# Optimization experiments

Measured on AMD Instinct MI355X. Metric: run time of the kernel, lower is better.

The kernel has to match this reference:

```python
import jax, jax.numpy as jnp
import numpy as np

N, E, F, H, L, G, C, NC = 100000, 1200000, 32, 64, 3, 256, 200000, 10
D = L * H  # concat node embedding dim = 192


def setup_inputs() -> dict:
    key = jax.random.key(0)
    ks = jax.random.split(key, 20)

    def w(k, shape):
        fan_in = shape[-2] if len(shape) > 1 else shape[0]
        return jax.random.normal(k, shape, jnp.float32) * (1.0 / np.sqrt(fan_in))

    inp = dict(
        x=jax.random.normal(ks[0], (N, F), jnp.float32),
        edge_index=jax.random.randint(ks[1], (2, E), 0, N),
        batch=jnp.sort(jax.random.randint(ks[2], (N,), 0, G)),
        cand_node=jax.random.randint(ks[3], (C,), 0, N),
        c1_W1=w(ks[4], (F, H)), c1_b1=jnp.zeros((H,)),
        c1_W2=w(ks[5], (H, H)), c1_b2=jnp.zeros((H,)),
        c1_g=jnp.ones((H,)), c1_be=jnp.zeros((H,)), c1_m=jnp.zeros((H,)), c1_v=jnp.ones((H,)),
        c1_eps=jnp.zeros((1,)),
        cs_W1=w(ks[6], (L - 1, H, H)), cs_b1=jnp.zeros((L - 1, H)),
        cs_W2=w(ks[7], (L - 1, H, H)), cs_b2=jnp.zeros((L - 1, H)),
        cs_g=jnp.ones((L - 1, H)), cs_be=jnp.zeros((L - 1, H)),
        cs_m=jnp.zeros((L - 1, H)), cs_v=jnp.ones((L - 1, H)),
        cs_eps=jnp.zeros((L - 1,)),
        nc_W1=w(ks[8], (D, 2 * H)), nc_b1=jnp.zeros((2 * H,)),
        nc_W2=w(ks[9], (2 * H, H)), nc_b2=jnp.zeros((H,)),
        nc_W3=w(ks[10], (H, H)), nc_b3=jnp.zeros((H,)),
        nc_W4=w(ks[11], (H, NC)), nc_b4=jnp.zeros((NC,)),
        comp_emb=jax.random.normal(ks[12], (NC, D), jnp.float32),
        ep_W1=w(ks[13], (2 * D, 2 * H)), ep_b1=jnp.zeros((2 * H,)),
        ep_W2=w(ks[14], (2 * H, H)), ep_b2=jnp.zeros((H,)),
        ep_W3=w(ks[15], (H, 1)), ep_b3=jnp.zeros((1,)),
    )
    return inp


def _bn(h, g, b, m, v):
    # BatchNorm1d in eval mode with running stats
    return g * (h - m) * jax.lax.rsqrt(v + 1e-5) + b


def _gin_layer(h, src, dst, eps, W1, b1, W2, b2, g, be, m, v):
    agg = jax.ops.segment_sum(h[src], dst, num_segments=N)  # sum aggregation
    h = (1.0 + eps) * h + agg
    h = jax.nn.relu(h @ W1 + b1)
    h = jax.nn.relu(h @ W2 + b2)
    return _bn(h, g, be, m, v)


def reference(x, edge_index, batch, cand_node,
              c1_W1, c1_b1, c1_W2, c1_b2, c1_g, c1_be, c1_m, c1_v, c1_eps,
              cs_W1, cs_b1, cs_W2, cs_b2, cs_g, cs_be, cs_m, cs_v, cs_eps,
              nc_W1, nc_b1, nc_W2, nc_b2, nc_W3, nc_b3, nc_W4, nc_b4,
              comp_emb, ep_W1, ep_b1, ep_W2, ep_b2, ep_W3, ep_b3):
    src, dst = edge_index[0], edge_index[1]
    # shared GIN encoder: concat per-layer node embeddings -> [N, L*H]
    h = _gin_layer(x, src, dst, c1_eps, c1_W1, c1_b1, c1_W2, c1_b2, c1_g, c1_be, c1_m, c1_v)
    xs = [h]
    for i in range(cs_W1.shape[0]):
        h = _gin_layer(h, src, dst, cs_eps[i], cs_W1[i], cs_b1[i], cs_W2[i], cs_b2[i],
                       cs_g[i], cs_be[i], cs_m[i], cs_v[i])
        xs.append(h)
    node_emb = jnp.concatenate(xs, axis=-1)  # [N, D]

    # global mean pool per graph -> classification head (dropout=identity in eval)
    sums = jax.ops.segment_sum(node_emb, batch, num_segments=G)
    cnt = jax.ops.segment_sum(jnp.ones((node_emb.shape[0], 1), node_emb.dtype), batch, num_segments=G)
    graph_emb = sums / jnp.maximum(cnt, 1.0)  # [G, D]
    hc = jax.nn.relu(graph_emb @ nc_W1 + nc_b1)
    hc = jax.nn.relu(hc @ nc_W2 + nc_b2)
    hc = jax.nn.relu(hc @ nc_W3 + nc_b3)
    logits = hc @ nc_W4 + nc_b4
    class_output = jax.nn.log_softmax(logits, axis=-1)  # [G, NC]

    # link prediction: predicted comp type per graph, score all candidates in one batch
    comp_idx = jnp.argmax(class_output, axis=-1)          # [G]
    cand_graph = batch[cand_node]                          # [C]
    ce = comp_emb[comp_idx[cand_graph]]                    # [C, D]
    de = node_emb[cand_node]                               # [C, D]
    ef = jnp.concatenate([ce, de], axis=-1)                # [C, 2D]
    he = jax.nn.relu(ef @ ep_W1 + ep_b1)
    he = jax.nn.relu(he @ ep_W2 + ep_b2)
    edge_scores = jax.nn.sigmoid((he @ ep_W3 + ep_b3).squeeze(-1))  # [C]
    return class_output, edge_scores
```

## Files before the change

### kernel.cpp

```cpp
#include <hip/hip_runtime.h>
#include <hip/hip_bf16.h>


#define GG 256
#define NCC 10
#define DD 192
#define BSH 9

#define PE_BLK 133
#define EN_BLK 88
#define XB_BLK 512

typedef short bf16x8 __attribute__((ext_vector_type(8)));
typedef float f32x4  __attribute__((ext_vector_type(4)));

__device__ inline unsigned short f2bf_u(float x) {
    __hip_bfloat16 h = __float2bfloat16(x);
    return *reinterpret_cast<unsigned short*>(&h);
}
__device__ inline float bf2f(unsigned short u) {
    return __uint_as_float(((unsigned int)u) << 16);
}

__global__ void prep_all(
    const float* __restrict__ epW1, const float* __restrict__ epb1,
    const float* __restrict__ epW2, const float* __restrict__ comp_emb,
    unsigned short* __restrict__ W1b_p, unsigned short* __restrict__ W2_p,
    float* __restrict__ pc,
    const float* __restrict__ c1W1, const float* __restrict__ c1W2,
    const float* __restrict__ csW1, const float* __restrict__ csW2,
    unsigned short* __restrict__ enc,
    const float* __restrict__ x, unsigned short* __restrict__ xb, int nx4,
    int* __restrict__ bcnt, int* __restrict__ nbrpad) {
    const int b = blockIdx.x, t = threadIdx.x;
    if (b < PE_BLK) {
        int idx = b * 256 + t;
        const int S1 = 6 * 8 * 512;
        const int S2 = 4 * 4 * 512;
        if (idx < S1) {
            int frag = idx >> 9;
            int lane = (idx >> 3) & 63;
            int j = idx & 7;
            int kstep = frag >> 3, nt = frag & 7;
            int k = kstep * 32 + ((lane >> 4) << 3) + j;
            int n = nt * 16 + (lane & 15);
            W1b_p[idx] = f2bf_u(epW1[(192 + k) * 128 + n]);
        } else if (idx < S1 + S2) {
            int i2 = idx - S1;
            int frag = i2 >> 9;
            int lane = (i2 >> 3) & 63;
            int j = i2 & 7;
            int kstep = frag >> 2, nt = frag & 3;
            int k = kstep * 32 + ((lane >> 4) << 3) + j;
            int n = nt * 16 + (lane & 15);
            W2_p[i2] = f2bf_u(epW2[k * 64 + n]);
        } else if (idx < S1 + S2 + NCC * 128) {
            int i3 = idx - (S1 + S2);
            int ci = i3 >> 7, col = i3 & 127;
            float a = epb1[col];
            for (int k = 0; k < DD; ++k) a += comp_emb[ci * DD + k] * epW1[k * 128 + col];
            pc[i3] = a;
        }
    } else if (b < PE_BLK + EN_BLK) {
        int idx = (b - PE_BLK) * 256 + t;
        if (idx < 22528) {
            const float* W; int rel;
            if (idx < 2048)       { W = c1W1;        rel = idx; }
            else if (idx < 6144)  { W = c1W2;        rel = idx - 2048; }
            else if (idx < 10240) { W = csW1;        rel = idx - 6144; }
            else if (idx < 14336) { W = csW2;        rel = idx - 10240; }
            else if (idx < 18432) { W = csW1 + 4096; rel = idx - 14336; }
            else                  { W = csW2 + 4096; rel = idx - 18432; }
            int frag = rel >> 9;
            int lane = (rel >> 3) & 63;
            int j = rel & 7;
            int ks = frag >> 2, nt = frag & 3;
            int k = ks * 32 + ((lane >> 4) << 3) + j;
            int n = nt * 16 + (lane & 15);
            enc[idx] = f2bf_u(W[k * 64 + n]);
        }
    } else if (b < PE_BLK + EN_BLK + XB_BLK) {
        for (int i = (b - PE_BLK - EN_BLK) * 256 + t; i < nx4; i += XB_BLK * 256) {
            float4 v = *(const float4*)(x + i * 4);
            ushort4 u;
            u.x = f2bf_u(v.x); u.y = f2bf_u(v.y); u.z = f2bf_u(v.z); u.w = f2bf_u(v.w);
            *(ushort4*)(xb + i * 4) = u;
        }
    } else {
        bcnt[t] = 0; bcnt[t + 256] = 0;
        if (t < 128) nbrpad[t] = 0;
    }
}

__global__ void bin_hist(const int* __restrict__ dst, int* __restrict__ bcnt, int E_) {
    __shared__ int h[512];
    const int t = threadIdx.x;
    h[t] = 0; h[t + 256] = 0;
    __syncthreads();
    for (int e = blockIdx.x * 256 + t; e < E_; e += gridDim.x * 256)
        atomicAdd(&h[dst[e] >> BSH], 1);
    __syncthreads();
    if (h[t]) atomicAdd(&bcnt[t], h[t]);
    if (h[t + 256]) atomicAdd(&bcnt[t + 256], h[t + 256]);
}

__global__ void scan_misc(const int* __restrict__ bcnt, int* __restrict__ bbase,
                          int* __restrict__ bpos, int NB, int E_,
                          const int* __restrict__ batch, int* __restrict__ gcnt_i,
                          float* __restrict__ gsum, int N_) {
    const int b = blockIdx.x, t = threadIdx.x;
    if (b == 0) {
        __shared__ int ps[256];
        int v0 = (2 * t < NB) ? bcnt[2 * t] : 0;
        int v1 = (2 * t + 1 < NB) ? bcnt[2 * t + 1] : 0;
        int pv = v0 + v1;
        ps[t] = pv;
        __syncthreads();
        for (int off = 1; off < 256; off <<= 1) {
            int x = (t >= off) ? ps[t - off] : 0;
            __syncthreads();
            ps[t] += x;
            __syncthreads();
        }
        const int excl = ps[t] - pv;
        if (2 * t < NB)     { bbase[2 * t] = excl;          bpos[2 * t] = excl; }
        if (2 * t + 1 < NB) { bbase[2 * t + 1] = excl + v0; bpos[2 * t + 1] = excl + v0; }
        if (t == 0) bbase[NB] = E_;
    } else if (b == 1) {
        __shared__ int lbs[GG + 1];
        int lo = 0, hi = N_;
        while (lo < hi) {
            int mid = (lo + hi) >> 1;
            if (batch[mid] < t) lo = mid + 1; else hi = mid;
        }
        lbs[t] = lo;
        if (t == 0) lbs[GG] = N_;
        __syncthreads();
        gcnt_i[t] = lbs[t + 1] - lbs[t];
    } else {
        int i = (b - 2) * 256 + t;
        if (i < GG * DD) gsum[i] = 0.f;
    }
}

__global__ __launch_bounds__(256) void bin_scatter(
    const int* __restrict__ src, const int* __restrict__ dst,
    int* __restrict__ bpos, unsigned* __restrict__ ebuf, int E_) {
    __shared__ int h[512];
    __shared__ int base[512];
    const int t = threadIdx.x;
    const int e0 = blockIdx.x * 4096;
    h[t] = 0; h[t + 256] = 0;
    __syncthreads();
    int myb[16], myr[16];
    unsigned pk[16];
    #pragma unroll
    for (int u = 0; u < 16; ++u) {
        int e = e0 + t + u * 256;
        if (e < E_) {
            int d = dst[e];
            myb[u] = d >> BSH;
            pk[u] = ((unsigned)src[e] << BSH) | (unsigned)(d & ((1 << BSH) - 1));
            myr[u] = atomicAdd(&h[myb[u]], 1);
        } else myb[u] = -1;
    }
    __syncthreads();
    if (h[t]) base[t] = atomicAdd(&bpos[t], h[t]);
    if (h[t + 256]) base[t + 256] = atomicAdd(&bpos[t + 256], h[t + 256]);
    __syncthreads();
    #pragma unroll
    for (int u = 0; u < 16; ++u)
        if (myb[u] >= 0)
            ebuf[base[myb[u]] + myr[u]] = pk[u];
}

__global__ __launch_bounds__(256) void csr_bucket(
    const unsigned* __restrict__ ebuf, const int* __restrict__ bbase,
    int* __restrict__ rowptr, int* __restrict__ nbr, int N_, int NB) {
    __shared__ int lh[512];
    __shared__ int lx[512];
    __shared__ int ps[256];
    const int b = blockIdx.x;
    const int t = threadIdx.x;
    const int ebase = bbase[b], eend = bbase[b + 1];
    const int ecnt = eend - ebase;
    const int n0 = b << BSH;
    const unsigned M = (1 << BSH) - 1;

    for (int i = t; i < 512; i += 256) lh[i] = 0;
    __syncthreads();
    for (int i = t; i < ecnt; i += 256)
        atomicAdd(&lh[ebuf[ebase + i] & M], 1);
    __syncthreads();

    int pv = lh[2 * t] + lh[2 * t + 1];
    ps[t] = pv;
    __syncthreads();
    for (int off = 1; off < 256; off <<= 1) {
        int x = (t >= off) ? ps[t - off] : 0;
        __syncthreads();
        ps[t] += x;
        __syncthreads();
    }
    const int excl = ps[t] - pv;
    lx[2 * t] = excl;
    lx[2 * t + 1] = excl + lh[2 * t];
    __syncthreads();

    for (int i = t; i < 512; i += 256) {
        int n = n0 + i;
        if (n < N_) rowptr[n] = ebase + lx[i];
    }
    if (b == NB - 1 && t == 0) rowptr[N_] = eend;
    __syncthreads();
    for (int i = t; i < 512; i += 256) lh[i] = lx[i];
    __syncthreads();
    for (int i = t; i < ecnt; i += 256) {
        unsigned p = ebuf[ebase + i];
        int r = atomicAdd(&lh[p & M], 1);
        nbr[ebase + r] = (int)(p >> BSH);
    }
}

#define SWZ(row, byte) ((byte) ^ (((row) & 7) << 4))

#define GSTEP(VCUR, VNXT)                                                     \
    _Pragma("unroll")                                                         \
    for (int u = 0; u < 16; ++u)                                              \
        VNXT[u] = bf2f(*(const unsigned short*)(hbase + (unsigned)idx[u] * (unsigned)RSB + lane2)); \
    _Pragma("unroll")                                                         \
    for (int u = 0; u < 16; ++u) idx[u] = nbp[k + 32 + u];                    \
    {                                                                         \
        float runk = run;                                                     \
        _Pragma("unroll")                                                     \
        for (int u = 0; u < 16; ++u) run += VCUR[u];                          \
        if ((unsigned)(e1 - k) < 16u) { float tt = runk;                      \
            _Pragma("unroll")                                                 \
            for (int u = 0; u < 16; ++u) tt += (u < e1 - k) ? VCUR[u] : 0.f;  \
            s0 = tt; }                                                        \
        if ((unsigned)(e2 - k) < 16u) { float tt = runk;                      \
            _Pragma("unroll")                                                 \
            for (int u = 0; u < 16; ++u) tt += (u < e2 - k) ? VCUR[u] : 0.f;  \
            s1 = tt; }                                                        \
        if ((unsigned)(e3 - k) < 16u) { float tt = runk;                      \
            _Pragma("unroll")                                                 \
            for (int u = 0; u < 16; ++u) tt += (u < e3 - k) ? VCUR[u] : 0.f;  \
            s2 = tt; }                                                        \
        if ((unsigned)(cnt - k) < 16u) { float tt = runk;                     \
            _Pragma("unroll")                                                 \
            for (int u = 0; u < 16; ++u) tt += (u < cnt - k) ? VCUR[u] : 0.f; \
            s3 = tt; }                                                        \
    }                                                                         \
    k += 16;                                                                  \
    if (k > cnt) break;

template<int K>
__global__ __launch_bounds__(512) void gin_fused(
    const unsigned short* __restrict__ hin_b,
    const int* __restrict__ rowptr, const int* __restrict__ nbr,
    const unsigned short* __restrict__ W1p, const float* __restrict__ b1,
    const unsigned short* __restrict__ W2p, const float* __restrict__ b2,
    const float* __restrict__ gamma, const float* __restrict__ beta,
    const float* __restrict__ mean, const float* __restrict__ var,
    const float* __restrict__ eps_p,
    __hip_bfloat16* __restrict__ out_b,
    const int* __restrict__ batch, float* __restrict__ gsum, int soff,
    int N_) {
    __shared__ char s_agg[32 * 128];
    __shared__ char s_h1[32 * 128];
    __shared__ char s_out[32 * 128];
    __shared__ int sb[32];

    const int t = threadIdx.x;
    const int lane = t & 63;
    const int w = t >> 6;
    const int node0 = blockIdx.x * 32;
    const int nb = w * 4;

    if (t < 32) sb[t] = (node0 + t < N_) ? batch[node0 + t] : -1;

    const float eps1 = 1.0f + eps_p[0];

    const int n0w = node0 + nb;
    const int rp0 = __builtin_amdgcn_readfirstlane(rowptr[min(n0w + 0, N_)]);
    const int rp1 = __builtin_amdgcn_readfirstlane(rowptr[min(n0w + 1, N_)]);
    const int rp2 = __builtin_amdgcn_readfirstlane(rowptr[min(n0w + 2, N_)]);
    const int rp3 = __builtin_amdgcn_readfirstlane(rowptr[min(n0w + 3, N_)]);
    const int rp4 = __builtin_amdgcn_readfirstlane(rowptr[min(n0w + 4, N_)]);
    const int cnt = rp4 - rp0;
    const int e1 = rp1 - rp0, e2 = rp2 - rp0, e3 = rp3 - rp0;
    const int* nbp = nbr + rp0;

    const int RSB = (K == 64) ? DD * 2 : 64;
    const int OST = (K == 64) ? DD : 32;
    const char* hbase = (const char*)hin_b;
    const unsigned lane2 = (unsigned)(lane & (K - 1)) * 2u;

    int idx[16];
    float vA[16], vB[16];
    float run = 0.f, s0 = 0.f, s1 = 0.f, s2 = 0.f, s3 = 0.f;
    #pragma unroll
    for (int u = 0; u < 16; ++u) idx[u] = nbp[u];
    #pragma unroll
    for (int u = 0; u < 16; ++u)
        vA[u] = bf2f(*(const unsigned short*)(hbase + (unsigned)idx[u] * (unsigned)RSB + lane2));
    #pragma unroll
    for (int u = 0; u < 16; ++u) idx[u] = nbp[16 + u];
    for (int k = 0;;) {
        GSTEP(vA, vB)
        GSTEP(vB, vA)
    }
    float a0 = s0, a1 = s1 - s0, a2 = s2 - s1, a3 = s3 - s2;
    {
        const unsigned short* hbp = hin_b + (lane & (K - 1));
        if (n0w + 0 < N_) a0 += eps1 * bf2f(hbp[(size_t)(n0w + 0) * OST]);
        if (n0w + 1 < N_) a1 += eps1 * bf2f(hbp[(size_t)(n0w + 1) * OST]);
        if (n0w + 2 < N_) a2 += eps1 * bf2f(hbp[(size_t)(n0w + 2) * OST]);
        if (n0w + 3 < N_) a3 += eps1 * bf2f(hbp[(size_t)(n0w + 3) * OST]);
    }
    if (K == 64 || lane < 32) {
        const int kd = lane & (K - 1);
        *(unsigned short*)(s_agg + SWZ(nb + 0, (nb + 0) * 128 + kd * 2)) = f2bf_u(a0);
        *(unsigned short*)(s_agg + SWZ(nb + 1, (nb + 1) * 128 + kd * 2)) = f2bf_u(a1);
        *(unsigned short*)(s_agg + SWZ(nb + 2, (nb + 2) * 128 + kd * 2)) = f2bf_u(a2);
        *(unsigned short*)(s_agg + SWZ(nb + 3, (nb + 3) * 128 + kd * 2)) = f2bf_u(a3);
    }
    __syncthreads();

    const int mt = w >> 2, nt = w & 3;
    const int arow = mt * 16 + (lane & 15);
    const int col = nt * 16 + (lane & 15);
    f32x4 c1v = (f32x4){0.f, 0.f, 0.f, 0.f};
    #pragma unroll
    for (int ks = 0; ks < K / 32; ++ks) {
        bf16x8 a = *(const bf16x8*)(s_agg + SWZ(arow, arow * 128 + ks * 64 + ((lane >> 4) << 4)));
        bf16x8 b = *(const bf16x8*)(W1p + (((ks << 2) + nt) << 9) + (lane << 3));
        c1v = __builtin_amdgcn_mfma_f32_16x16x32_bf16(a, b, c1v, 0, 0, 0);
    }
    {
        const float bb1 = b1[col];
        #pragma unroll
        for (int reg = 0; reg < 4; ++reg) {
            int row = mt * 16 + ((lane >> 4) << 2) + reg;
            float v = fmaxf(c1v[reg] + bb1, 0.f);
            *(unsigned short*)(s_h1 + SWZ(row, row * 128 + col * 2)) = f2bf_u(v);
        }
    }
    __syncthreads();

    f32x4 c2v = (f32x4){0.f, 0.f, 0.f, 0.f};
    #pragma unroll
    for (int ks = 0; ks < 2; ++ks) {
        bf16x8 a = *(const bf16x8*)(s_h1 + SWZ(arow, arow * 128 + ks * 64 + ((lane >> 4) << 4)));
        bf16x8 b = *(const bf16x8*)(W2p + (((ks << 2) + nt) << 9) + (lane << 3));
        c2v = __builtin_amdgcn_mfma_f32_16x16x32_bf16(a, b, c2v, 0, 0, 0);
    }
    {
        const float bb2 = b2[col];
        const float ga = gamma[col], bet = beta[col], mu = mean[col];
        const float iv = rsqrtf(var[col] + 1e-5f);
        #pragma unroll
        for (int reg = 0; reg < 4; ++reg) {
            int row = mt * 16 + ((lane >> 4) << 2) + reg;
            float v = fmaxf(c2v[reg] + bb2, 0.f);
            v = ga * (v - mu) * iv + bet;
            *(unsigned short*)(s_out + SWZ(row, row * 128 + col * 2)) = f2bf_u(v);
        }
    }
    __syncthreads();

    {
        int r = t >> 4, c8 = t & 15;
        int node = node0 + r;
        if (node < N_) {
            ushort4 v = *(const ushort4*)(s_out + SWZ(r, r * 128 + c8 * 8));
            *(ushort4*)((unsigned short*)out_b + (size_t)node * DD + c8 * 4) = v;
        }
    }

    if (t < 256) {
        const int d = t & 63;
        const int rg = t >> 6;
        float acc = 0.f;
        int curg = sb[rg * 8];
        #pragma unroll
        for (int r = rg * 8; r < rg * 8 + 8; ++r) {
            int g = sb[r];
            if (g != curg) {
                if (curg >= 0) atomicAdd(&gsum[curg * DD + soff + d], acc);
                acc = 0.f; curg = g;
            }
            if (g >= 0)
                acc += bf2f(*(const unsigned short*)(s_out + SWZ(r, r * 128 + d * 2)));
        }
        if (curg >= 0) atomicAdd(&gsum[curg * DD + soff + d], acc);
    }
}

__global__ void head_kernel(const float* __restrict__ gsum, const int* __restrict__ gcnt_i,
                            const float* __restrict__ W1, const float* __restrict__ b1,
                            const float* __restrict__ W2, const float* __restrict__ b2,
                            const float* __restrict__ W3, const float* __restrict__ b3,
                            const float* __restrict__ W4, const float* __restrict__ b4,
                            float* __restrict__ class_out, int* __restrict__ comp_idx) {
    const int g = blockIdx.x;
    const int t = threadIdx.x;
    __shared__ float ge[DD], h1[128], h2[64], h3[64], logits[NCC];

    const float c = fmaxf((float)gcnt_i[g], 1.0f);
    if (t < DD) ge[t] = gsum[g * DD + t] / c;
    __syncthreads();

    if (t < 128) {
        float a = b1[t];
        #pragma unroll 4
        for (int k = 0; k < DD; ++k) a += ge[k] * W1[k * 128 + t];
        h1[t] = fmaxf(a, 0.0f);
    }
    __syncthreads();
    if (t < 64) {
        float a = b2[t];
        #pragma unroll 4
        for (int k = 0; k < 128; ++k) a += h1[k] * W2[k * 64 + t];
        h2[t] = fmaxf(a, 0.0f);
    }
    __syncthreads();
    if (t < 64) {
        float a = b3[t];
        #pragma unroll 4
        for (int k = 0; k < 64; ++k) a += h2[k] * W3[k * 64 + t];
        h3[t] = fmaxf(a, 0.0f);
    }
    __syncthreads();
    if (t < NCC) {
        float a = b4[t];
        #pragma unroll
        for (int k = 0; k < 64; ++k) a += h3[k] * W4[k * NCC + t];
        logits[t] = a;
    }
    __syncthreads();
    if (t == 0) {
        float mx = logits[0]; int am = 0;
        for (int j = 1; j < NCC; ++j) if (logits[j] > mx) { mx = logits[j]; am = j; }
        float se = 0.0f;
        for (int j = 0; j < NCC; ++j) se += expf(logits[j] - mx);
        float lse = logf(se);
        for (int j = 0; j < NCC; ++j) class_out[g * NCC + j] = logits[j] - mx - lse;
        comp_idx[g] = am;
    }
}

__global__ __launch_bounds__(256, 5) void edge_mfma(
    const int* __restrict__ cand, const int* __restrict__ batch,
    const int* __restrict__ comp_idx, const short* __restrict__ hb,
    const unsigned short* __restrict__ W1b_p, const unsigned short* __restrict__ W2_p,
    const float* __restrict__ pc, const float* __restrict__ W3,
    const float* __restrict__ b3, float* __restrict__ scores, int C_) {
    __shared__ char s_buf[64 * 384];
    __shared__ float s_part[4][64];
    __shared__ int s_node[64];
    __shared__ int s_ci[64];
    __shared__ float s_w3[64];

    const int t = threadIdx.x;
    const int lane = t & 63;
    const int w = t >> 6;
    const int c0 = blockIdx.x * 64;

    if (t < 64) {
        int c = c0 + t;
        int node = (c < C_) ? cand[c] : cand[0];
        s_node[t] = node;
        s_ci[t] = comp_idx[batch[node]];
        s_w3[t] = W3[t];
    }
    __syncthreads();

    for (int i = t; i < 64 * 24; i += 256) {
        int r = i / 24, c8 = i - r * 24;
        bf16x8 v = *(const bf16x8*)(hb + (size_t)s_node[r] * DD + c8 * 8);
        *(bf16x8*)(s_buf + SWZ(r, r * 384 + c8 * 16)) = v;
    }
    __syncthreads();

    f32x4 acc1[4][2];
    #pragma unroll
    for (int rt = 0; rt < 4; ++rt)
        #pragma unroll
        for (int b = 0; b < 2; ++b) acc1[rt][b] = (f32x4){0.f, 0.f, 0.f, 0.f};
    #pragma unroll
    for (int ks = 0; ks < 6; ++ks) {
        bf16x8 b0 = *(const bf16x8*)(W1b_p + ((ks * 8 + 2 * w + 0) << 9) + (lane << 3));
        bf16x8 b1f = *(const bf16x8*)(W1b_p + ((ks * 8 + 2 * w + 1) << 9) + (lane << 3));
        #pragma unroll
        for (int rt = 0; rt < 4; ++rt) {
            int arow = rt * 16 + (lane & 15);
            bf16x8 a = *(const bf16x8*)(s_buf + SWZ(arow, arow * 384 + ks * 64 + ((lane >> 4) << 4)));
            acc1[rt][0] = __builtin_amdgcn_mfma_f32_16x16x32_bf16(a, b0, acc1[rt][0], 0, 0, 0);
            acc1[rt][1] = __builtin_amdgcn_mfma_f32_16x16x32_bf16(a, b1f, acc1[rt][1], 0, 0, 0);
        }
    }
    __syncthreads();

    #pragma unroll
    for (int rt = 0; rt < 4; ++rt) {
        #pragma unroll
        for (int reg = 0; reg < 4; ++reg) {
            int row = rt * 16 + ((lane >> 4) << 2) + reg;
            int ci = s_ci[row];
            #pragma unroll
            for (int b = 0; b < 2; ++b) {
                int col = (2 * w + b) * 16 + (lane & 15);
                float v = fmaxf(acc1[rt][b][reg] + pc[ci * 128 + col], 0.f);
                *(unsigned short*)(s_buf + SWZ(row, row * 256 + col * 2)) = f2bf_u(v);
            }
        }
    }
    __syncthreads();

    f32x4 acc2[4];
    #pragma unroll
    for (int rt = 0; rt < 4; ++rt) acc2[rt] = (f32x4){0.f, 0.f, 0.f, 0.f};
    #pragma unroll
    for (int ks = 0; ks < 4; ++ks) {
        bf16x8 b = *(const bf16x8*)(W2_p + ((ks * 4 + w) << 9) + (lane << 3));
        #pragma unroll
        for (int rt = 0; rt < 4; ++rt) {
            int arow = rt * 16 + (lane & 15);
            bf16x8 a = *(const bf16x8*)(s_buf + SWZ(arow, arow * 256 + ks * 64 + ((lane >> 4) << 4)));
            acc2[rt] = __builtin_amdgcn_mfma_f32_16x16x32_bf16(a, b, acc2[rt], 0, 0, 0);
        }
    }

    {
        const float w3v = s_w3[w * 16 + (lane & 15)];
        #pragma unroll
        for (int rt = 0; rt < 4; ++rt) {
            #pragma unroll
            for (int reg = 0; reg < 4; ++reg) {
                float p = fmaxf(acc2[rt][reg], 0.f) * w3v;
                p += __shfl_xor(p, 1);
                p += __shfl_xor(p, 2);
                p += __shfl_xor(p, 4);
                p += __shfl_xor(p, 8);
                if ((lane & 15) == 0)
                    s_part[w][rt * 16 + ((lane >> 4) << 2) + reg] = p;
            }
        }
    }
    __syncthreads();

    if (t < 64) {
        int c = c0 + t;
        if (c < C_) {
            float p = s_part[0][t] + s_part[1][t] + s_part[2][t] + s_part[3][t] + b3[0];
            scores[c] = 1.0f / (1.0f + expf(-p));
        }
    }
}

extern "C" void kernel_launch(void* const* d_in, const int* in_sizes, int n_in,
                              void* d_out, int out_size, void* d_ws, size_t ws_size,
                              hipStream_t stream) {
    const float* x        = (const float*)d_in[0];
    const int*   ei       = (const int*)d_in[1];
    const int*   batch    = (const int*)d_in[2];
    const int*   cand     = (const int*)d_in[3];
    const float* c1_W1    = (const float*)d_in[4];
    const float* c1_b1    = (const float*)d_in[5];
    const float* c1_W2    = (const float*)d_in[6];
    const float* c1_b2    = (const float*)d_in[7];
    const float* c1_g     = (const float*)d_in[8];
    const float* c1_be    = (const float*)d_in[9];
    const float* c1_m     = (const float*)d_in[10];
    const float* c1_v     = (const float*)d_in[11];
    const float* c1_eps   = (const float*)d_in[12];
    const float* cs_W1    = (const float*)d_in[13];
    const float* cs_b1    = (const float*)d_in[14];
    const float* cs_W2    = (const float*)d_in[15];
    const float* cs_b2    = (const float*)d_in[16];
    const float* cs_g     = (const float*)d_in[17];
    const float* cs_be    = (const float*)d_in[18];
    const float* cs_m     = (const float*)d_in[19];
    const float* cs_v     = (const float*)d_in[20];
    const float* cs_eps   = (const float*)d_in[21];
    const float* nc_W1    = (const float*)d_in[22];
    const float* nc_b1    = (const float*)d_in[23];
    const float* nc_W2    = (const float*)d_in[24];
    const float* nc_b2    = (const float*)d_in[25];
    const float* nc_W3    = (const float*)d_in[26];
    const float* nc_b3    = (const float*)d_in[27];
    const float* nc_W4    = (const float*)d_in[28];
    const float* nc_b4    = (const float*)d_in[29];
    const float* comp_emb = (const float*)d_in[30];
    const float* ep_W1    = (const float*)d_in[31];
    const float* ep_b1    = (const float*)d_in[32];
    const float* ep_W2    = (const float*)d_in[33];
    const float* ep_b2    = (const float*)d_in[34];
    const float* ep_W3    = (const float*)d_in[35];
    const float* ep_b3    = (const float*)d_in[36];

    const int N_ = in_sizes[0] / 32;
    const int E_ = in_sizes[1] / 2;
    const int C_ = in_sizes[3];
    const int* src = ei;
    const int* dst = ei + E_;
    const int NB = (N_ + (1 << BSH) - 1) >> BSH;

    char* ws = (char*)d_ws;
    size_t off = 0;
    __hip_bfloat16* hb = (__hip_bfloat16*)(ws + off); off += (size_t)N_ * DD * 2;
    unsigned short* xb = (unsigned short*)(ws + off); off += (size_t)N_ * 32 * 2;
    int*   rowptr   = (int*)(ws + off);   off += (size_t)(N_ + 2) * 4;
    int*   nbr      = (int*)(ws + off);   off += (size_t)(E_ + 128) * 4;
    int*   bcnt     = (int*)(ws + off);   off += 2048;
    int*   bbase    = (int*)(ws + off);   off += 2080;
    int*   bpos     = (int*)(ws + off);   off += 2048;
    float* gsum     = (float*)(ws + off); off += (size_t)GG * DD * 4;
    int*   gcnt_i   = (int*)(ws + off);   off += 1024;
    int*   comp_idx = (int*)(ws + off);   off += 1024;
    float* pc       = (float*)(ws + off); off += NCC * 128 * 4;
    unsigned short* W1b_p = (unsigned short*)(ws + off); off += 6 * 8 * 512 * 2;
    unsigned short* W2_p  = (unsigned short*)(ws + off); off += 4 * 4 * 512 * 2;
    unsigned short* enc   = (unsigned short*)(ws + off); off += 22528 * 2;
    unsigned* ebuf  = (unsigned*)hb;

    float* class_out = (float*)d_out;
    float* scores    = class_out + GG * NCC;

    prep_all<<<PE_BLK + EN_BLK + XB_BLK + 1, 256, 0, stream>>>(
        ep_W1, ep_b1, ep_W2, comp_emb, W1b_p, W2_p, pc,
        c1_W1, c1_W2, cs_W1, cs_W2, enc,
        x, xb, N_ * 32 / 4, bcnt, nbr + E_);

    bin_hist<<<256, 256, 0, stream>>>(dst, bcnt, E_);
    scan_misc<<<2 + (GG * DD + 255) / 256, 256, 0, stream>>>(
        bcnt, bbase, bpos, NB, E_, batch, gcnt_i, gsum, N_);
    bin_scatter<<<(E_ + 4095) / 4096, 256, 0, stream>>>(src, dst, bpos, ebuf, E_);
    csr_bucket<<<NB, 256, 0, stream>>>(ebuf, bbase, rowptr, nbr, N_, NB);

    const int gblk = (N_ + 31) / 32;
    gin_fused<32><<<gblk, 512, 0, stream>>>(
        xb, rowptr, nbr,
        enc + 0, c1_b1, enc + 2048, c1_b2,
        c1_g, c1_be, c1_m, c1_v, c1_eps, hb + 0, batch, gsum, 0, N_);
    gin_fused<64><<<gblk, 512, 0, stream>>>(
        (const unsigned short*)hb + 0, rowptr, nbr,
        enc + 6144, cs_b1 + 0, enc + 10240, cs_b2 + 0,
        cs_g + 0, cs_be + 0, cs_m + 0, cs_v + 0, cs_eps + 0, hb + 64, batch, gsum, 64, N_);
    gin_fused<64><<<gblk, 512, 0, stream>>>(
        (const unsigned short*)hb + 64, rowptr, nbr,
        enc + 14336, cs_b1 + 64, enc + 18432, cs_b2 + 64,
        cs_g + 64, cs_be + 64, cs_m + 64, cs_v + 64, cs_eps + 1, hb + 128, batch, gsum, 128, N_);

    head_kernel<<<GG, 256, 0, stream>>>(gsum, gcnt_i, nc_W1, nc_b1, nc_W2, nc_b2,
                                        nc_W3, nc_b3, nc_W4, nc_b4, class_out, comp_idx);

    edge_mfma<<<(C_ + 63) / 64, 256, 0, stream>>>(
        cand, batch, comp_idx, (const short*)hb, W1b_p, W2_p, pc, ep_W3, ep_b3, scores, C_);
}
```

Baseline: 249.2 us.

## Fold bin histogram into prep kernel with per-block partials; widen csr_bucket to 512 threads

The separate bin_hist launch goes away. Its work moves into 64 extra blocks of prep_all, and each of those blocks writes its own partial histogram instead of using global atomics. scan_misc then sums the 64 partials before its prefix scan, which also removes the need to zero bcnt first. csr_bucket runs with 512 threads so each thread owns one node slot and the scan covers all 512 entries directly. The aim is to save a kernel launch and the global atomic contention, at the cost of a serial partial reduction in scan block 0 and fewer blocks doing the histogram.

```diff
diff --git a/kernel.cpp b/kernel.cpp
--- a/kernel.cpp
+++ b/kernel.cpp
@@ -10,6 +10,7 @@
 #define PE_BLK 133
 #define EN_BLK 88
 #define XB_BLK 512
+#define HI_BLK 64
 
 typedef short bf16x8 __attribute__((ext_vector_type(8)));
 typedef float f32x4  __attribute__((ext_vector_type(4)));
@@ -31,7 +32,8 @@
     const float* __restrict__ csW1, const float* __restrict__ csW2,
     unsigned short* __restrict__ enc,
     const float* __restrict__ x, unsigned short* __restrict__ xb, int nx4,
-    int* __restrict__ bcnt, int* __restrict__ nbrpad) {
+    const int* __restrict__ dst, int E_, int* __restrict__ hist_part,
+    int* __restrict__ nbrpad) {
     const int b = blockIdx.x, t = threadIdx.x;
     if (b < PE_BLK) {
         int idx = b * 256 + t;
@@ -86,33 +88,34 @@
             u.x = f2bf_u(v.x); u.y = f2bf_u(v.y); u.z = f2bf_u(v.z); u.w = f2bf_u(v.w);
             *(ushort4*)(xb + i * 4) = u;
         }
+    } else if (b < PE_BLK + EN_BLK + XB_BLK + HI_BLK) {
+        __shared__ int h[512];
+        const int hbk = b - (PE_BLK + EN_BLK + XB_BLK);
+        h[t] = 0; h[t + 256] = 0;
+        __syncthreads();
+        for (int e = hbk * 256 + t; e < E_; e += HI_BLK * 256)
+            atomicAdd(&h[dst[e] >> BSH], 1);
+        __syncthreads();
+        hist_part[hbk * 512 + t] = h[t];
+        hist_part[hbk * 512 + t + 256] = h[t + 256];
     } else {
-        bcnt[t] = 0; bcnt[t + 256] = 0;
         if (t < 128) nbrpad[t] = 0;
     }
 }
 
-__global__ void bin_hist(const int* __restrict__ dst, int* __restrict__ bcnt, int E_) {
-    __shared__ int h[512];
-    const int t = threadIdx.x;
-    h[t] = 0; h[t + 256] = 0;
-    __syncthreads();
-    for (int e = blockIdx.x * 256 + t; e < E_; e += gridDim.x * 256)
-        atomicAdd(&h[dst[e] >> BSH], 1);
-    __syncthreads();
-    if (h[t]) atomicAdd(&bcnt[t], h[t]);
-    if (h[t + 256]) atomicAdd(&bcnt[t + 256], h[t + 256]);
-}
-
-__global__ void scan_misc(const int* __restrict__ bcnt, int* __restrict__ bbase,
+__global__ void scan_misc(const int* __restrict__ hist_part, int* __restrict__ bbase,
                           int* __restrict__ bpos, int NB, int E_,
                           const int* __restrict__ batch, int* __restrict__ gcnt_i,
                           float* __restrict__ gsum, int N_) {
     const int b = blockIdx.x, t = threadIdx.x;
     if (b == 0) {
         __shared__ int ps[256];
-        int v0 = (2 * t < NB) ? bcnt[2 * t] : 0;
-        int v1 = (2 * t + 1 < NB) ? bcnt[2 * t + 1] : 0;
+        int v0 = 0, v1 = 0;
+        #pragma unroll 4
+        for (int p = 0; p < HI_BLK; ++p) {
+            v0 += hist_part[p * 512 + 2 * t];
+            v1 += hist_part[p * 512 + 2 * t + 1];
+        }
         int pv = v0 + v1;
         ps[t] = pv;
         __syncthreads();
@@ -174,12 +177,11 @@
             ebuf[base[myb[u]] + myr[u]] = pk[u];
 }
 
-__global__ __launch_bounds__(256) void csr_bucket(
+__global__ __launch_bounds__(512) void csr_bucket(
     const unsigned* __restrict__ ebuf, const int* __restrict__ bbase,
     int* __restrict__ rowptr, int* __restrict__ nbr, int N_, int NB) {
     __shared__ int lh[512];
     __shared__ int lx[512];
-    __shared__ int ps[256];
     const int b = blockIdx.x;
     const int t = threadIdx.x;
     const int ebase = bbase[b], eend = bbase[b + 1];
@@ -187,35 +189,31 @@
     const int n0 = b << BSH;
     const unsigned M = (1 << BSH) - 1;
 
-    for (int i = t; i < 512; i += 256) lh[i] = 0;
-    __syncthreads();
-    for (int i = t; i < ecnt; i += 256)
+    lh[t] = 0;
+    __syncthreads();
+    for (int i = t; i < ecnt; i += 512)
         atomicAdd(&lh[ebuf[ebase + i] & M], 1);
     __syncthreads();
 
-    int pv = lh[2 * t] + lh[2 * t + 1];
-    ps[t] = pv;
-    __syncthreads();
-    for (int off = 1; off < 256; off <<= 1) {
-        int x = (t >= off) ? ps[t - off] : 0;
+    int v = lh[t];
+    lx[t] = v;
+    __syncthreads();
+    for (int off = 1; off < 512; off <<= 1) {
+        int x = (t >= off) ? lx[t - off] : 0;
         __syncthreads();
-        ps[t] += x;
+        lx[t] += x;
         __syncthreads();
     }
-    const int excl = ps[t] - pv;
-    lx[2 * t] = excl;
-    lx[2 * t + 1] = excl + lh[2 * t];
-    __syncthreads();
-
-    for (int i = t; i < 512; i += 256) {
-        int n = n0 + i;
-        if (n < N_) rowptr[n] = ebase + lx[i];
+    const int excl = lx[t] - v;
+    {
+        int n = n0 + t;
+        if (n < N_) rowptr[n] = ebase + excl;
     }
     if (b == NB - 1 && t == 0) rowptr[N_] = eend;
     __syncthreads();
-    for (int i = t; i < 512; i += 256) lh[i] = lx[i];
-    __syncthreads();
-    for (int i = t; i < ecnt; i += 256) {
+    lh[t] = excl;
+    __syncthreads();
+    for (int i = t; i < ecnt; i += 512) {
         unsigned p = ebuf[ebase + i];
         int r = atomicAdd(&lh[p & M], 1);
         nbr[ebase + r] = (int)(p >> BSH);
@@ -613,7 +611,7 @@
     unsigned short* xb = (unsigned short*)(ws + off); off += (size_t)N_ * 32 * 2;
     int*   rowptr   = (int*)(ws + off);   off += (size_t)(N_ + 2) * 4;
     int*   nbr      = (int*)(ws + off);   off += (size_t)(E_ + 128) * 4;
-    int*   bcnt     = (int*)(ws + off);   off += 2048;
+    int*   hist_part= (int*)(ws + off);   off += (size_t)HI_BLK * 512 * 4;
     int*   bbase    = (int*)(ws + off);   off += 2080;
     int*   bpos     = (int*)(ws + off);   off += 2048;
     float* gsum     = (float*)(ws + off); off += (size_t)GG * DD * 4;
@@ -628,16 +626,15 @@
     float* class_out = (float*)d_out;
     float* scores    = class_out + GG * NCC;
 
-    prep_all<<<PE_BLK + EN_BLK + XB_BLK + 1, 256, 0, stream>>>(
+    prep_all<<<PE_BLK + EN_BLK + XB_BLK + HI_BLK + 1, 256, 0, stream>>>(
         ep_W1, ep_b1, ep_W2, comp_emb, W1b_p, W2_p, pc,
         c1_W1, c1_W2, cs_W1, cs_W2, enc,
-        x, xb, N_ * 32 / 4, bcnt, nbr + E_);
-
-    bin_hist<<<256, 256, 0, stream>>>(dst, bcnt, E_);
+        x, xb, N_ * 32 / 4, dst, E_, hist_part, nbr + E_);
+
     scan_misc<<<2 + (GG * DD + 255) / 256, 256, 0, stream>>>(
-        bcnt, bbase, bpos, NB, E_, batch, gcnt_i, gsum, N_);
+        hist_part, bbase, bpos, NB, E_, batch, gcnt_i, gsum, N_);
     bin_scatter<<<(E_ + 4095) / 4096, 256, 0, stream>>>(src, dst, bpos, ebuf, E_);
-    csr_bucket<<<NB, 256, 0, stream>>>(ebuf, bbase, rowptr, nbr, N_, NB);
+    csr_bucket<<<NB, 512, 0, stream>>>(ebuf, bbase, rowptr, nbr, N_, NB);
 
     const int gblk = (N_ + 31) / 32;
     gin_fused<32><<<gblk, 512, 0, stream>>>(
```

After: 246.2 us, median of 2. Within noise of the previous version (-1.2%).
